# Kernel tuning notes

Measured on AMD Instinct MI355X. Metric: run time of the kernel, lower is better.

## Reference

```python
import jax, jax.numpy as jnp
import numpy as np

EPS = 1e-5

def _inst_norm(x):
    # mean-variance normalization per (batch, channel) over spatial dims
    mu = jnp.mean(x, axis=(2, 3), keepdims=True)
    var = jnp.var(x, axis=(2, 3), keepdims=True)
    return (x - mu) / jnp.sqrt(var + EPS)

def _conv1x1(x, w, b):
    # x: (B,C,H,W), w: (O,C), b: (O,)
    return jnp.einsum('bchw,oc->bohw', x, w) + b[None, :, None, None]

def setup_inputs() -> dict:
    key = jax.random.key(0)
    ks = jax.random.split(key, 8)
    B, C, H, W = 16, 512, 64, 64
    f_c = jax.random.normal(ks[0], (B, C, H, W), dtype=jnp.float32)
    f_s = jax.random.normal(ks[1], (B, C, H, W), dtype=jnp.float32)
    w1 = jax.random.normal(ks[2], (C, C), dtype=jnp.float32) * 0.02
    b1 = jax.random.normal(ks[3], (C,), dtype=jnp.float32) * 0.02
    w2 = jax.random.normal(ks[4], (C, C), dtype=jnp.float32) * 0.02
    b2 = jax.random.normal(ks[5], (C,), dtype=jnp.float32) * 0.02
    w3 = jax.random.normal(ks[6], (C, C), dtype=jnp.float32) * 0.02
    b3 = jax.random.normal(ks[7], (C,), dtype=jnp.float32) * 0.02
    return {"f_c": f_c, "f_s": f_s, "w1": w1, "b1": b1, "w2": w2, "b2": b2, "w3": w3, "b3": b3}

def reference(f_c, f_s, w1, b1, w2, b2, w3, b3):
    b, c, h, w = f_c.shape
    f_c_norm = _inst_norm(f_c)
    f_s_norm = _inst_norm(f_s)
    fc = _conv1x1(f_c_norm, w1, b1).reshape(b, c, h * w)  # (B,C,HW)
    gs = _conv1x1(f_s_norm, w2, b2).reshape(b, c, h * w)  # (B,C,HW)
    hs = _conv1x1(f_s, w3, b3).reshape(b, c, h * w)       # (B,C,HW)
    # channel attention map (B,C,C) — softmax-free
    attn = jnp.einsum('bcn,bdn->bcd', gs, fc)
    out = jnp.einsum('bcd,bdn->bcn', attn, hs)
    return out.reshape(b, c, h, w)
```

## Files before the change

kernel.cpp:

```cpp
#include <hip/hip_runtime.h>
#include <hip/hip_bf16.h>

typedef float f4 __attribute__((ext_vector_type(4)));
typedef __bf16 bf16x4 __attribute__((ext_vector_type(4)));
typedef __bf16 bf16x8 __attribute__((ext_vector_type(8)));

#define BATCH 16
#define CCH 512
#define HW 4096

__global__ __launch_bounds__(256) void stats_conv_kernel(
    const float* __restrict__ fc, const float* __restrict__ fs,
    __bf16* __restrict__ fcb, __bf16* __restrict__ fsb,
    float* __restrict__ rstd_c, float* __restrict__ rmu_c,
    float* __restrict__ rstd_s, float* __restrict__ rmu_s)
{
    const int row = blockIdx.x;
    const bool is_c = (blockIdx.y == 0);
    const float* src = (is_c ? fc : fs) + (size_t)row * HW;
    __bf16* dst = is_c ? fcb : fsb;
    float s = 0.f, sq = 0.f;
    for (int i = threadIdx.x; i < HW / 4; i += 256) {
        f4 v = ((const f4*)src)[i];
        s  += v[0] + v[1] + v[2] + v[3];
        sq += v[0]*v[0] + v[1]*v[1] + v[2]*v[2] + v[3]*v[3];
        if (dst) {
            bf16x4 o;
            o[0] = (__bf16)v[0]; o[1] = (__bf16)v[1]; o[2] = (__bf16)v[2]; o[3] = (__bf16)v[3];
            *(bf16x4*)(dst + (size_t)row * HW + i * 4) = o;
        }
    }
    for (int off = 32; off > 0; off >>= 1) {
        s  += __shfl_down(s,  off, 64);
        sq += __shfl_down(sq, off, 64);
    }
    __shared__ float ss[4], ssq[4];
    if ((threadIdx.x & 63) == 0) { ss[threadIdx.x >> 6] = s; ssq[threadIdx.x >> 6] = sq; }
    __syncthreads();
    if (threadIdx.x == 0) {
        float S = ss[0] + ss[1] + ss[2] + ss[3];
        float Q = ssq[0] + ssq[1] + ssq[2] + ssq[3];
        float mu  = S * (1.f / HW);
        float var = Q * (1.f / HW) - mu * mu;
        float r = rsqrtf(var + 1e-5f);
        (is_c ? rstd_c : rstd_s)[row] = r;
        (is_c ? rmu_c  : rmu_s )[row] = r * mu;
    }
}

__global__ __launch_bounds__(256) void prep_w_kernel(
    const float* __restrict__ w1, const float* __restrict__ w2, const float* __restrict__ w3,
    __bf16* __restrict__ w1t, __bf16* __restrict__ w2b, __bf16* __restrict__ w3t)
{
    int i = blockIdx.x * 256 + threadIdx.x;
    int z = blockIdx.y;
    if (z == 0)      w2b[i] = (__bf16)w2[i];
    else if (z == 1) w3t[i] = (__bf16)w3[(i & 511) * 512 + (i >> 9)];
    else             w1t[i] = (__bf16)w1[(i & 511) * 512 + (i >> 9)];
}

__global__ __launch_bounds__(256) void u_kernel(
    const float* __restrict__ w1, const float* __restrict__ b3,
    const float* __restrict__ w3, const float* __restrict__ b1,
    float* __restrict__ u1, float* __restrict__ bw3)
{
    int d = blockIdx.x * 256 + threadIdx.x;
    const float* W = blockIdx.y == 0 ? w1 : w3;
    const float* v = blockIdx.y == 0 ? b3 : b1;
    float* o       = blockIdx.y == 0 ? u1 : bw3;
    float s = 0.f;
    for (int x = 0; x < 512; x++) s += W[x * 512 + d] * v[x];
    o[d] = s;
}

__global__ __launch_bounds__(256) void b1b3_kernel(
    const float* __restrict__ b1, const float* __restrict__ b3, float* __restrict__ o)
{
    int t = threadIdx.x;
    float s = b1[t] * b3[t] + b1[t + 256] * b3[t + 256];
    for (int off = 32; off > 0; off >>= 1) s += __shfl_down(s, off, 64);
    __shared__ float ss[4];
    if ((t & 63) == 0) ss[t >> 6] = s;
    __syncthreads();
    if (t == 0) o[0] = ss[0] + ss[1] + ss[2] + ss[3];
}

__global__ __launch_bounds__(256) void gram_epi_kernel(
    const float* __restrict__ Graw, __bf16* __restrict__ G,
    const float* __restrict__ rstd_s, const float* __restrict__ rmu_s,
    const float* __restrict__ rstd_c, const float* __restrict__ rmu_c)
{
    size_t i4 = (size_t)blockIdx.x * 256 + threadIdx.x;
    size_t flat = i4 * 4;
    int b  = (int)(flat >> 18);
    int c  = (int)((flat >> 9) & 511);
    int d0 = (int)(flat & 511);
    float rs = rstd_s[b * 512 + c], rm = rmu_s[b * 512 + c];
    f4 g = *(const f4*)(Graw + flat);
    bf16x4 o;
    #pragma unroll
    for (int t = 0; t < 4; t++) {
        float val = rs * rstd_c[b * 512 + d0 + t] * g[t]
                  - 4096.f * rm * rmu_c[b * 512 + d0 + t];
        o[t] = (__bf16)val;
    }
    *(bf16x4*)(G + flat) = o;
}

__global__ __launch_bounds__(64) void q_kernel(
    const __bf16* __restrict__ G, const float* __restrict__ u1, float* __restrict__ q)
{
    int r = blockIdx.x;
    const __bf16* row = G + (size_t)r * 512;
    float s = 0.f;
    for (int i = threadIdx.x; i < 512; i += 64) s += (float)row[i] * u1[i];
    for (int off = 32; off > 0; off >>= 1) s += __shfl_down(s, off, 64);
    if (threadIdx.x == 0) q[r] = s;
}

__global__ __launch_bounds__(64) void v2_kernel(
    const float* __restrict__ w2, const float* __restrict__ qv,
    const float* __restrict__ b2, const float* __restrict__ b1b3,
    float* __restrict__ vv)
{
    int r = blockIdx.x, b = r >> 9, c = r & 511;
    float s = 0.f;
    for (int i = threadIdx.x; i < 512; i += 64) s += w2[c * 512 + i] * qv[b * 512 + i];
    for (int off = 32; off > 0; off >>= 1) s += __shfl_down(s, off, 64);
    if (threadIdx.x == 0) vv[r] = s + 4096.f * b1b3[0] * b2[c];
}

template<int BM, int BN, bool A_F32, bool B_F32, bool B_KMAJOR, bool D_F32, bool ATOMIC>
__global__ __launch_bounds__(256) void gemm_kernel(
    const void* __restrict__ Ap, const void* __restrict__ Bp, void* __restrict__ Dp,
    int K, int splitk, int lda, int ldb, int ldd,
    long long sA, long long sB, long long sD,
    const float* __restrict__ s1, int vs1, const float* __restrict__ s2, int vs2,
    const float* __restrict__ t1, int vt1, const float* __restrict__ t2, int vt2,
    float tscale)
{
    static_assert(B_KMAJOR || BN == 128, "NN staging assumes BN=128");
    constexpr int FM = BM / 32, FN = BN / 32;
    constexpr int LSA = 40;
    constexpr int LSB = B_KMAJOR ? 40 : 36;
    __shared__ __bf16 As[BM * LSA];
    __shared__ __bf16 Bs[BN * LSB];

    const int tid = threadIdx.x;
    const int b = blockIdx.z / splitk;
    const int chunk = blockIdx.z % splitk;
    const int klen = K / splitk;
    const int k0 = chunk * klen, k1 = k0 + klen;
    const int m0 = blockIdx.y * BM, n0 = blockIdx.x * BN;
    const int lane = tid & 63, wid = tid >> 6;
    const int wm = (wid >> 1) * (BM / 2), wn = (wid & 1) * (BN / 2);
    const int l16 = lane & 15, l4 = lane >> 4;

    const char* Abase = (const char*)Ap + (long long)b * sA * (A_F32 ? 4 : 2);
    const char* Bbase = (const char*)Bp + (long long)b * sB * (B_F32 ? 4 : 2);
    char* Dbase = (char*)Dp + (long long)b * sD * (D_F32 ? 4 : 2);

    f4 acc[FM][FN];
    #pragma unroll
    for (int i = 0; i < FM; i++)
        #pragma unroll
        for (int j = 0; j < FN; j++) acc[i][j] = (f4){0.f, 0.f, 0.f, 0.f};

    for (int kt = k0; kt < k1; kt += 32) {
        __syncthreads();
        if (A_F32) {
            const float* A32 = (const float*)Abase;
            #pragma unroll
            for (int it = 0; it < BM / 32; it++) {
                int q = it * 256 + tid;
                int r = q >> 3, c = (q & 7) * 4;
                f4 v = *(const f4*)(A32 + (size_t)(m0 + r) * lda + kt + c);
                bf16x4 o;
                o[0] = (__bf16)v[0]; o[1] = (__bf16)v[1]; o[2] = (__bf16)v[2]; o[3] = (__bf16)v[3];
                *(bf16x4*)&As[r * LSA + c] = o;
            }
        } else {
            const __bf16* A16 = (const __bf16*)Abase;
            #pragma unroll
            for (int it = 0; it < BM / 64; it++) {
                int q = it * 256 + tid;
                int r = q >> 2, c = (q & 3) * 8;
                *(bf16x8*)&As[r * LSA + c] = *(const bf16x8*)(A16 + (size_t)(m0 + r) * lda + kt + c);
            }
        }
        if (B_KMAJOR) {
            if (B_F32) {
                const float* B32 = (const float*)Bbase;
                #pragma unroll
                for (int it = 0; it < BN / 32; it++) {
                    int q = it * 256 + tid;
                    int r = q >> 3, c = (q & 7) * 4;
                    f4 v = *(const f4*)(B32 + (size_t)(n0 + r) * ldb + kt + c);
                    bf16x4 o;
                    o[0] = (__bf16)v[0]; o[1] = (__bf16)v[1]; o[2] = (__bf16)v[2]; o[3] = (__bf16)v[3];
                    *(bf16x4*)&Bs[r * LSB + c] = o;
                }
            } else {
                const __bf16* B16 = (const __bf16*)Bbase;
                #pragma unroll
                for (int it = 0; it < BN / 64; it++) {
                    int q = it * 256 + tid;
                    int r = q >> 2, c = (q & 3) * 8;
                    *(bf16x8*)&Bs[r * LSB + c] = *(const bf16x8*)(B16 + (size_t)(n0 + r) * ldb + kt + c);
                }
            }
        } else {
            const int n = tid & 127;
            const int kh = (tid >> 7) * 4;
            #pragma unroll
            for (int kk = 0; kk < 32; kk += 8) {
                int k = kk + kh;
                bf16x4 o;
                if (B_F32) {
                    const float* B32 = (const float*)Bbase;
                    #pragma unroll
                    for (int t = 0; t < 4; t++)
                        o[t] = (__bf16)B32[(size_t)(kt + k + t) * ldb + n0 + n];
                } else {
                    const __bf16* B16 = (const __bf16*)Bbase;
                    #pragma unroll
                    for (int t = 0; t < 4; t++)
                        o[t] = B16[(size_t)(kt + k + t) * ldb + n0 + n];
                }
                *(bf16x4*)&Bs[n * LSB + k] = o;
            }
        }
        __syncthreads();

        bf16x8 af[FM], bfr[FN];
        #pragma unroll
        for (int i = 0; i < FM; i++)
            af[i] = *(const bf16x8*)&As[(wm + i * 16 + l16) * LSA + l4 * 8];
        #pragma unroll
        for (int j = 0; j < FN; j++) {
            if (B_KMAJOR) {
                bfr[j] = *(const bf16x8*)&Bs[(wn + j * 16 + l16) * LSB + l4 * 8];
            } else {
                const __bf16* p = &Bs[(wn + j * 16 + l16) * LSB + l4 * 8];
                bf16x4 lo = *(const bf16x4*)p;
                bf16x4 hi = *(const bf16x4*)(p + 4);
                bf16x8 r;
                r[0]=lo[0]; r[1]=lo[1]; r[2]=lo[2]; r[3]=lo[3];
                r[4]=hi[0]; r[5]=hi[1]; r[6]=hi[2]; r[7]=hi[3];
                bfr[j] = r;
            }
        }
        #pragma unroll
        for (int i = 0; i < FM; i++)
            #pragma unroll
            for (int j = 0; j < FN; j++)
                acc[i][j] = __builtin_amdgcn_mfma_f32_16x16x32_bf16(af[i], bfr[j], acc[i][j], 0, 0, 0);
    }

    if (ATOMIC) {
        float* D32 = (float*)Dbase;
        #pragma unroll
        for (int j = 0; j < FN; j++) {
            int col = n0 + wn + j * 16 + l16;
            #pragma unroll
            for (int i = 0; i < FM; i++)
                #pragma unroll
                for (int rr = 0; rr < 4; rr++) {
                    int row = m0 + wm + i * 16 + l4 * 4 + rr;
                    atomicAdd(D32 + (size_t)row * ldd + col, acc[i][j][rr]);
                }
        }
        return;
    }
    const float* s1b = s1 ? s1 + (long long)b * vs1 : nullptr;
    const float* s2b = s2 ? s2 + (long long)b * vs2 : nullptr;
    const float* t1b = t1 ? t1 + (long long)b * vt1 : nullptr;
    const float* t2b = t2 ? t2 + (long long)b * vt2 : nullptr;
    #pragma unroll
    for (int j = 0; j < FN; j++) {
        int col = n0 + wn + j * 16 + l16;
        float cs = s2b ? s2b[col] : 1.f;
        float ct = t2b ? t2b[col] : 1.f;
        #pragma unroll
        for (int i = 0; i < FM; i++) {
            #pragma unroll
            for (int rr = 0; rr < 4; rr++) {
                int row = m0 + wm + i * 16 + l4 * 4 + rr;
                float val = acc[i][j][rr];
                if (s1b) val *= s1b[row];
                val *= cs;
                if (t1b) val += tscale * t1b[row] * ct;
                size_t idx = (size_t)row * ldd + col;
                if (D_F32) ((float*)Dbase)[idx] = val;
                else       ((__bf16*)Dbase)[idx] = (__bf16)val;
            }
        }
    }
}

extern "C" void kernel_launch(void* const* d_in, const int* in_sizes, int n_in,
                              void* d_out, int out_size, void* d_ws, size_t ws_size,
                              hipStream_t stream) {
    (void)in_sizes; (void)n_in; (void)out_size;
    const float* f_c = (const float*)d_in[0];
    const float* f_s = (const float*)d_in[1];
    const float* w1  = (const float*)d_in[2];
    const float* b1  = (const float*)d_in[3];
    const float* w2  = (const float*)d_in[4];
    const float* b2  = (const float*)d_in[5];
    const float* w3  = (const float*)d_in[6];
    const float* b3  = (const float*)d_in[7];
    float* out = (float*)d_out;

    char* ws = (char*)d_ws;
    float*  rstd_c = (float*)(ws + 0);
    float*  rmu_c  = (float*)(ws + 32768);
    float*  rstd_s = (float*)(ws + 65536);
    float*  rmu_s  = (float*)(ws + 98304);
    float*  vvec   = (float*)(ws + 131072);
    float*  qvec   = (float*)(ws + 163840);
    float*  u1     = (float*)(ws + 196608);
    float*  bw3    = (float*)(ws + 198656);
    float*  b1b3p  = (float*)(ws + 200704);
    __bf16* w2b    = (__bf16*)(ws + 262144);
    __bf16* w1t    = (__bf16*)(ws + 786432);
    __bf16* w3t    = (__bf16*)(ws + 1310720);
    __bf16* w13t   = (__bf16*)(ws + 1835008);
    float*  Graw   = (float*)(ws + 2359296);
    __bf16* Pt     = (__bf16*)(ws + 2359296);
    __bf16* Mbuf   = (__bf16*)(ws + 10747904);
    __bf16* G      = (__bf16*)(ws + 19136512);
    __bf16* fcb    = (__bf16*)(ws + 27525120);
    __bf16* fsb    = (__bf16*)(ws + 94633984);
    const bool CONV = ws_size >= (size_t)161742848;

    const long long sBig = (long long)CCH * HW;
    const long long sSm  = (long long)CCH * CCH;

    stats_conv_kernel<<<dim3(BATCH * CCH, 2), 256, 0, stream>>>(
        f_c, f_s, CONV ? fcb : nullptr, CONV ? fsb : nullptr,
        rstd_c, rmu_c, rstd_s, rmu_s);
    prep_w_kernel<<<dim3(1024, 3), 256, 0, stream>>>(w1, w2, w3, w1t, w2b, w3t);
    u_kernel<<<dim3(2, 2), 256, 0, stream>>>(w1, b3, w3, b1, u1, bw3);
    b1b3_kernel<<<1, 256, 0, stream>>>(b1, b3, b1b3p);
    (void)hipMemsetAsync(Graw, 0, (size_t)16777216, stream);

    if (CONV)
        gemm_kernel<128,128,false,false,true,true,true><<<dim3(4, 4, BATCH * 4), 256, 0, stream>>>(
            fsb, fcb, Graw, HW, 4, HW, HW, CCH, sBig, sBig, sSm,
            nullptr,0, nullptr,0, nullptr,0, nullptr,0, 0.f);
    else
        gemm_kernel<128,128,true,true,true,true,true><<<dim3(4, 4, BATCH * 4), 256, 0, stream>>>(
            f_s, f_c, Graw, HW, 4, HW, HW, CCH, sBig, sBig, sSm,
            nullptr,0, nullptr,0, nullptr,0, nullptr,0, 0.f);
    gram_epi_kernel<<<4096, 256, 0, stream>>>(Graw, G, rstd_s, rmu_s, rstd_c, rmu_c);

    gemm_kernel<64,64,false,false,true,false,false><<<dim3(8, 8, 1), 256, 0, stream>>>(
        w3t, w1t, w13t, CCH, 1, CCH, CCH, CCH, 0, 0, 0,
        nullptr,0, nullptr,0, nullptr,0, nullptr,0, 0.f);
    gemm_kernel<64,64,false,false,true,false,false><<<dim3(8, 8, BATCH), 256, 0, stream>>>(
        w13t, G, Pt, CCH, 1, CCH, CCH, CCH, 0, sSm, sSm,
        nullptr,0, nullptr,0, nullptr,0, nullptr,0, 0.f);
    gemm_kernel<64,64,false,false,true,false,false><<<dim3(8, 8, BATCH), 256, 0, stream>>>(
        w2b, Pt, Mbuf, CCH, 1, CCH, CCH, CCH, 0, sSm, sSm,
        nullptr,0, nullptr,0, b2,0, bw3,0, 4096.f);

    q_kernel<<<BATCH * CCH, 64, 0, stream>>>(G, u1, qvec);
    v2_kernel<<<BATCH * CCH, 64, 0, stream>>>(w2, qvec, b2, b1b3p, vvec);

    if (CONV)
        gemm_kernel<128,128,false,false,false,true,false><<<dim3(32, 4, BATCH), 256, 0, stream>>>(
            Mbuf, fsb, out, CCH, 1, CCH, HW, HW, sSm, sBig, sBig,
            nullptr,0, nullptr,0, vvec,CCH, nullptr,0, 1.f);
    else
        gemm_kernel<128,128,false,true,false,true,false><<<dim3(32, 4, BATCH), 256, 0, stream>>>(
            Mbuf, f_s, out, CCH, 1, CCH, HW, HW, sSm, sBig, sBig,
            nullptr,0, nullptr,0, vvec,CCH, nullptr,0, 1.f);
}
```

Before: 625.0 us.

## Add direct global-to-LDS NT GEMM, fuse stats passes, transpose fs for final GEMM

Adds a new bf16 NT GEMM that loads tiles straight into LDS with global_load_lds and uses an XOR-swizzled layout. It replaces the gram GEMM, the two small per-batch GEMMs (now 128x128 tiles) and the final output GEMM. For the final GEMM it first transposes the bf16 f_s copy into a K-major buffer placed where fcb lived, so every GEMM runs in NT form. The stats kernel now handles f_c and f_s in one block with 8-wide vector loads and stores, halving launches. The extra transpose pass adds memory traffic, and reusing the fcb region assumes fcb is no longer needed after the gram GEMM.

```diff
diff --git a/kernel.cpp b/kernel.cpp
--- a/kernel.cpp
+++ b/kernel.cpp
@@ -8,6 +8,12 @@
 #define BATCH 16
 #define CCH 512
 #define HW 4096
+
+__device__ __forceinline__ void gld_lds16(const void* g, void* l) {
+    __builtin_amdgcn_global_load_lds(
+        (const __attribute__((address_space(1))) unsigned int*)g,
+        (__attribute__((address_space(3))) unsigned int*)l, 16, 0, 0);
+}
 
 __global__ __launch_bounds__(256) void stats_conv_kernel(
     const float* __restrict__ fc, const float* __restrict__ fs,
@@ -16,35 +22,54 @@
     float* __restrict__ rstd_s, float* __restrict__ rmu_s)
 {
     const int row = blockIdx.x;
-    const bool is_c = (blockIdx.y == 0);
-    const float* src = (is_c ? fc : fs) + (size_t)row * HW;
-    __bf16* dst = is_c ? fcb : fsb;
-    float s = 0.f, sq = 0.f;
-    for (int i = threadIdx.x; i < HW / 4; i += 256) {
-        f4 v = ((const f4*)src)[i];
-        s  += v[0] + v[1] + v[2] + v[3];
-        sq += v[0]*v[0] + v[1]*v[1] + v[2]*v[2] + v[3]*v[3];
-        if (dst) {
-            bf16x4 o;
-            o[0] = (__bf16)v[0]; o[1] = (__bf16)v[1]; o[2] = (__bf16)v[2]; o[3] = (__bf16)v[3];
-            *(bf16x4*)(dst + (size_t)row * HW + i * 4) = o;
+    const float* pc = fc + (size_t)row * HW;
+    const float* ps = fs + (size_t)row * HW;
+    float sc = 0.f, qc = 0.f, ssum = 0.f, qs = 0.f;
+    #pragma unroll
+    for (int i0 = 0; i0 < HW / 8 / 256; i0++) {
+        int i = i0 * 256 + threadIdx.x;
+        f4 a0 = ((const f4*)pc)[2 * i], a1 = ((const f4*)pc)[2 * i + 1];
+        f4 b0 = ((const f4*)ps)[2 * i], b1 = ((const f4*)ps)[2 * i + 1];
+        #pragma unroll
+        for (int t = 0; t < 4; t++) {
+            sc += a0[t] + a1[t];
+            qc = fmaf(a0[t], a0[t], fmaf(a1[t], a1[t], qc));
+            ssum += b0[t] + b1[t];
+            qs = fmaf(b0[t], b0[t], fmaf(b1[t], b1[t], qs));
+        }
+        if (fcb) {
+            bf16x8 oa, ob;
+            #pragma unroll
+            for (int t = 0; t < 4; t++) {
+                oa[t] = (__bf16)a0[t]; oa[4 + t] = (__bf16)a1[t];
+                ob[t] = (__bf16)b0[t]; ob[4 + t] = (__bf16)b1[t];
+            }
+            *(bf16x8*)(fcb + (size_t)row * HW + i * 8) = oa;
+            *(bf16x8*)(fsb + (size_t)row * HW + i * 8) = ob;
         }
     }
     for (int off = 32; off > 0; off >>= 1) {
-        s  += __shfl_down(s,  off, 64);
-        sq += __shfl_down(sq, off, 64);
-    }
-    __shared__ float ss[4], ssq[4];
-    if ((threadIdx.x & 63) == 0) { ss[threadIdx.x >> 6] = s; ssq[threadIdx.x >> 6] = sq; }
+        sc   += __shfl_down(sc,   off, 64);
+        qc   += __shfl_down(qc,   off, 64);
+        ssum += __shfl_down(ssum, off, 64);
+        qs   += __shfl_down(qs,   off, 64);
+    }
+    __shared__ float red[4][4];
+    if ((threadIdx.x & 63) == 0) {
+        int w = threadIdx.x >> 6;
+        red[w][0] = sc; red[w][1] = qc; red[w][2] = ssum; red[w][3] = qs;
+    }
     __syncthreads();
     if (threadIdx.x == 0) {
-        float S = ss[0] + ss[1] + ss[2] + ss[3];
-        float Q = ssq[0] + ssq[1] + ssq[2] + ssq[3];
-        float mu  = S * (1.f / HW);
-        float var = Q * (1.f / HW) - mu * mu;
-        float r = rsqrtf(var + 1e-5f);
-        (is_c ? rstd_c : rstd_s)[row] = r;
-        (is_c ? rmu_c  : rmu_s )[row] = r * mu;
+        float Sc = red[0][0] + red[1][0] + red[2][0] + red[3][0];
+        float Qc = red[0][1] + red[1][1] + red[2][1] + red[3][1];
+        float Ss = red[0][2] + red[1][2] + red[2][2] + red[3][2];
+        float Qs = red[0][3] + red[1][3] + red[2][3] + red[3][3];
+        float muc = Sc * (1.f / HW), varc = Qc * (1.f / HW) - muc * muc;
+        float mus = Ss * (1.f / HW), vars = Qs * (1.f / HW) - mus * mus;
+        float rc = rsqrtf(varc + 1e-5f), rs = rsqrtf(vars + 1e-5f);
+        rstd_c[row] = rc; rmu_c[row] = rc * muc;
+        rstd_s[row] = rs; rmu_s[row] = rs * mus;
     }
 }
 
@@ -128,6 +153,137 @@
     for (int i = threadIdx.x; i < 512; i += 64) s += w2[c * 512 + i] * qv[b * 512 + i];
     for (int off = 32; off > 0; off >>= 1) s += __shfl_down(s, off, 64);
     if (threadIdx.x == 0) vv[r] = s + 4096.f * b1b3[0] * b2[c];
+}
+
+__global__ __launch_bounds__(256) void transpose_kernel(
+    const __bf16* __restrict__ in, __bf16* __restrict__ out)
+{
+    __shared__ __align__(16) __bf16 t[64 * 64];
+    const int b = blockIdx.z, e0 = blockIdx.y * 64, n0 = blockIdx.x * 64;
+    const int tid = threadIdx.x;
+    const __bf16* src = in + ((size_t)b * 512 + e0) * HW + n0;
+    __bf16* dst = out + ((size_t)b * HW + n0) * 512 + e0;
+    #pragma unroll
+    for (int it = 0; it < 2; it++) {
+        int idx = it * 256 + tid;
+        int e = idx >> 3, v = idx & 7;
+        *(bf16x8*)&t[e * 64 + ((v ^ (e & 7)) * 8)] =
+            *(const bf16x8*)(src + (size_t)e * HW + v * 8);
+    }
+    __syncthreads();
+    #pragma unroll
+    for (int it = 0; it < 2; it++) {
+        int idx = it * 256 + tid;
+        int n = idx >> 3, v = idx & 7;
+        bf16x8 o;
+        #pragma unroll
+        for (int u = 0; u < 8; u++) {
+            int row = v * 8 + u;
+            o[u] = t[row * 64 + (((n >> 3) ^ u) * 8) + (n & 7)];
+        }
+        *(bf16x8*)(dst + (size_t)n * 512 + v * 8) = o;
+    }
+}
+
+template<int BM, int BN, bool D_F32, bool ATOMIC>
+__global__ __launch_bounds__(256) void gemm_nt_lds(
+    const __bf16* __restrict__ A, const __bf16* __restrict__ B, void* __restrict__ D,
+    int K, int splitk, int lda, int ldb, int ldd,
+    long long sA, long long sB, long long sD,
+    const float* __restrict__ t1, int vt1, const float* __restrict__ t2, int vt2,
+    float tscale)
+{
+    constexpr int FM = BM / 32, FN = BN / 32;
+    __shared__ __align__(16) __bf16 As[BM * 64];
+    __shared__ __align__(16) __bf16 Bs[BN * 64];
+
+    const int tid = threadIdx.x;
+    const int lane = tid & 63, wid = tid >> 6;
+    const int b = blockIdx.z / splitk, chunk = blockIdx.z % splitk;
+    const int klen = K / splitk, k0 = chunk * klen, k1 = k0 + klen;
+    const int m0 = blockIdx.y * BM, n0 = blockIdx.x * BN;
+    const int l16 = lane & 15, l4 = lane >> 4;
+    const int wm = (wid >> 1) * (BM / 2), wn = (wid & 1) * (BN / 2);
+    const int r_in = lane >> 3, slot = lane & 7;
+    const int csw = (slot ^ r_in) * 8;
+    const int rsw = (l16 & 7) * 8;
+
+    const __bf16* Ab = A + (long long)b * sA;
+    const __bf16* Bb = B + (long long)b * sB;
+
+    f4 acc[FM][FN];
+    #pragma unroll
+    for (int i = 0; i < FM; i++)
+        #pragma unroll
+        for (int j = 0; j < FN; j++) acc[i][j] = (f4){0.f, 0.f, 0.f, 0.f};
+
+    for (int kt = k0; kt < k1; kt += 64) {
+        __syncthreads();
+        #pragma unroll
+        for (int i = 0; i < BM / 32; i++) {
+            int ch = i * 4 + wid;
+            gld_lds16(Ab + (long long)(m0 + ch * 8 + r_in) * lda + kt + csw,
+                      As + ch * 512);
+        }
+        #pragma unroll
+        for (int i = 0; i < BN / 32; i++) {
+            int ch = i * 4 + wid;
+            gld_lds16(Bb + (long long)(n0 + ch * 8 + r_in) * ldb + kt + csw,
+                      Bs + ch * 512);
+        }
+        __syncthreads();
+        #pragma unroll
+        for (int kk = 0; kk < 2; kk++) {
+            bf16x8 af[FM], bfr[FN];
+            #pragma unroll
+            for (int i = 0; i < FM; i++)
+                af[i] = *(const bf16x8*)&As[(wm + i * 16 + l16) * 64 + ((kk * 32 + l4 * 8) ^ rsw)];
+            #pragma unroll
+            for (int j = 0; j < FN; j++)
+                bfr[j] = *(const bf16x8*)&Bs[(wn + j * 16 + l16) * 64 + ((kk * 32 + l4 * 8) ^ rsw)];
+            #pragma unroll
+            for (int i = 0; i < FM; i++)
+                #pragma unroll
+                for (int j = 0; j < FN; j++)
+                    acc[i][j] = __builtin_amdgcn_mfma_f32_16x16x32_bf16(af[i], bfr[j], acc[i][j], 0, 0, 0);
+        }
+    }
+
+    char* Dbase = (char*)D + (long long)b * sD * (D_F32 ? 4 : 2);
+    if (ATOMIC) {
+        float* D32 = (float*)Dbase;
+        #pragma unroll
+        for (int j = 0; j < FN; j++) {
+            int col = n0 + wn + j * 16 + l16;
+            #pragma unroll
+            for (int i = 0; i < FM; i++)
+                #pragma unroll
+                for (int rr = 0; rr < 4; rr++) {
+                    int row = m0 + wm + i * 16 + l4 * 4 + rr;
+                    atomicAdd(D32 + (size_t)row * ldd + col, acc[i][j][rr]);
+                }
+        }
+        return;
+    }
+    const float* t1b = t1 ? t1 + (long long)b * vt1 : nullptr;
+    const float* t2b = t2 ? t2 + (long long)b * vt2 : nullptr;
+    #pragma unroll
+    for (int j = 0; j < FN; j++) {
+        int col = n0 + wn + j * 16 + l16;
+        float ct = t2b ? t2b[col] : 1.f;
+        #pragma unroll
+        for (int i = 0; i < FM; i++) {
+            #pragma unroll
+            for (int rr = 0; rr < 4; rr++) {
+                int row = m0 + wm + i * 16 + l4 * 4 + rr;
+                float val = acc[i][j][rr];
+                if (t1b) val += tscale * t1b[row] * ct;
+                size_t idx = (size_t)row * ldd + col;
+                if (D_F32) ((float*)Dbase)[idx] = val;
+                else       ((__bf16*)Dbase)[idx] = (__bf16)val;
+            }
+        }
+    }
 }
 
 template<int BM, int BN, bool A_F32, bool B_F32, bool B_KMAJOR, bool D_F32, bool ATOMIC>
@@ -331,13 +487,14 @@
     __bf16* Mbuf   = (__bf16*)(ws + 10747904);
     __bf16* G      = (__bf16*)(ws + 19136512);
     __bf16* fcb    = (__bf16*)(ws + 27525120);
+    __bf16* fst    = (__bf16*)(ws + 27525120);
     __bf16* fsb    = (__bf16*)(ws + 94633984);
     const bool CONV = ws_size >= (size_t)161742848;
 
     const long long sBig = (long long)CCH * HW;
     const long long sSm  = (long long)CCH * CCH;
 
-    stats_conv_kernel<<<dim3(BATCH * CCH, 2), 256, 0, stream>>>(
+    stats_conv_kernel<<<dim3(BATCH * CCH), 256, 0, stream>>>(
         f_c, f_s, CONV ? fcb : nullptr, CONV ? fsb : nullptr,
         rstd_c, rmu_c, rstd_s, rmu_s);
     prep_w_kernel<<<dim3(1024, 3), 256, 0, stream>>>(w1, w2, w3, w1t, w2b, w3t);
@@ -346,32 +503,35 @@
     (void)hipMemsetAsync(Graw, 0, (size_t)16777216, stream);
 
     if (CONV)
-        gemm_kernel<128,128,false,false,true,true,true><<<dim3(4, 4, BATCH * 4), 256, 0, stream>>>(
+        gemm_nt_lds<128, 128, true, true><<<dim3(4, 4, BATCH * 4), 256, 0, stream>>>(
             fsb, fcb, Graw, HW, 4, HW, HW, CCH, sBig, sBig, sSm,
-            nullptr,0, nullptr,0, nullptr,0, nullptr,0, 0.f);
+            nullptr, 0, nullptr, 0, 0.f);
     else
         gemm_kernel<128,128,true,true,true,true,true><<<dim3(4, 4, BATCH * 4), 256, 0, stream>>>(
             f_s, f_c, Graw, HW, 4, HW, HW, CCH, sBig, sBig, sSm,
             nullptr,0, nullptr,0, nullptr,0, nullptr,0, 0.f);
     gram_epi_kernel<<<4096, 256, 0, stream>>>(Graw, G, rstd_s, rmu_s, rstd_c, rmu_c);
 
+    if (CONV)
+        transpose_kernel<<<dim3(64, 8, BATCH), 256, 0, stream>>>(fsb, fst);
+
     gemm_kernel<64,64,false,false,true,false,false><<<dim3(8, 8, 1), 256, 0, stream>>>(
         w3t, w1t, w13t, CCH, 1, CCH, CCH, CCH, 0, 0, 0,
         nullptr,0, nullptr,0, nullptr,0, nullptr,0, 0.f);
-    gemm_kernel<64,64,false,false,true,false,false><<<dim3(8, 8, BATCH), 256, 0, stream>>>(
+    gemm_nt_lds<128, 128, false, false><<<dim3(4, 4, BATCH), 256, 0, stream>>>(
         w13t, G, Pt, CCH, 1, CCH, CCH, CCH, 0, sSm, sSm,
-        nullptr,0, nullptr,0, nullptr,0, nullptr,0, 0.f);
-    gemm_kernel<64,64,false,false,true,false,false><<<dim3(8, 8, BATCH), 256, 0, stream>>>(
+        nullptr, 0, nullptr, 0, 0.f);
+    gemm_nt_lds<128, 128, false, false><<<dim3(4, 4, BATCH), 256, 0, stream>>>(
         w2b, Pt, Mbuf, CCH, 1, CCH, CCH, CCH, 0, sSm, sSm,
-        nullptr,0, nullptr,0, b2,0, bw3,0, 4096.f);
+        b2, 0, bw3, 0, 4096.f);
 
     q_kernel<<<BATCH * CCH, 64, 0, stream>>>(G, u1, qvec);
     v2_kernel<<<BATCH * CCH, 64, 0, stream>>>(w2, qvec, b2, b1b3p, vvec);
 
     if (CONV)
-        gemm_kernel<128,128,false,false,false,true,false><<<dim3(32, 4, BATCH), 256, 0, stream>>>(
-            Mbuf, fsb, out, CCH, 1, CCH, HW, HW, sSm, sBig, sBig,
-            nullptr,0, nullptr,0, vvec,CCH, nullptr,0, 1.f);
+        gemm_nt_lds<128, 128, true, false><<<dim3(32, 4, BATCH), 256, 0, stream>>>(
+            Mbuf, fst, out, CCH, 1, CCH, CCH, HW, sSm, sBig, sBig,
+            vvec, CCH, nullptr, 0, 1.f);
     else
         gemm_kernel<128,128,false,true,false,true,false><<<dim3(32, 4, BATCH), 256, 0, stream>>>(
             Mbuf, f_s, out, CCH, 1, CCH, HW, HW, sSm, sBig, sBig,
```

Result: no change. 627.4 us (+0.4%).
